# Optimization experiments

Hardware: AMD Instinct MI355X
Metric: run time of the kernel (lower is better)

The kernel has to match this reference:

```python
import jax, jax.numpy as jnp
import numpy as np

NUM_BANDS, B, K, D = 5, 512, 64, 200
H = 4            # num attention heads
HID = 512        # selector hidden width
S = 0.02         # weight init scale


def setup_inputs() -> dict:
    key = jax.random.key(0)
    ks = jax.random.split(key, 8)
    F_IN = NUM_BANDS * K * D  # 64000
    return {
        "bands": jax.random.normal(ks[0], (NUM_BANDS, B, K, D), jnp.float32),
        "w1": jax.random.normal(ks[1], (HID, F_IN), jnp.float32) * S,
        "b1": jnp.zeros((HID,), jnp.float32),
        "w2": jax.random.normal(ks[2], (NUM_BANDS, HID), jnp.float32) * S,
        "b2": jnp.zeros((NUM_BANDS,), jnp.float32),
        "in_proj_w": jax.random.normal(ks[3], (3 * D, D), jnp.float32) * S,
        "in_proj_b": jnp.zeros((3 * D,), jnp.float32),
        "out_w": jax.random.normal(ks[4], (D, D), jnp.float32) * S,
        "out_b": jnp.zeros((D,), jnp.float32),
    }


def reference(bands, w1, b1, w2, b2, in_proj_w, in_proj_b, out_w, out_b):
    nb, Bb, k, d = bands.shape
    hd = d // H
    scale = 1.0 / np.sqrt(hd)

    # concat(bands, dim=1): [B, nb*k, d] in band-major order
    x = jnp.transpose(bands, (1, 0, 2, 3))           # [B, nb, k, d]
    kv_in = x.reshape(Bb, nb * k, d)                 # [B, nb*k, d]

    # router MLP + softmax + argmax band select
    flat = kv_in.reshape(Bb, -1)                     # [B, nb*k*d]
    h = jax.nn.relu(flat @ w1.T + b1)                # [B, HID]
    band_weights = jax.nn.softmax(h @ w2.T + b2, axis=-1)
    sel = jnp.argmax(band_weights, axis=-1)          # [B] int

    # gather selected band per sample as the query
    Q = bands[sel, jnp.arange(Bb)]                   # [B, k, d]

    # multihead cross-attention (torch nn.MultiheadAttention math)
    wq, wk, wv = jnp.split(in_proj_w, 3, axis=0)
    bq, bk, bv = jnp.split(in_proj_b, 3, axis=0)
    q = (Q @ wq.T + bq).reshape(Bb, k, H, hd).transpose(0, 2, 1, 3)        # [B,H,k,hd]
    kk = (kv_in @ wk.T + bk).reshape(Bb, nb * k, H, hd).transpose(0, 2, 1, 3)
    v = (kv_in @ wv.T + bv).reshape(Bb, nb * k, H, hd).transpose(0, 2, 1, 3)

    attn = jax.nn.softmax(jnp.einsum('bhqe,bhke->bhqk', q, kk) * scale, axis=-1)
    o = jnp.einsum('bhqk,bhke->bhqe', attn, v)       # [B,H,k,hd]
    o = o.transpose(0, 2, 1, 3).reshape(Bb, k, d)
    return o @ out_w.T + out_b                        # [B, k, d]
```

## Files before the change

### kernel.cpp

```cpp
#include <hip/hip_runtime.h>
#include <hip/hip_bf16.h>

#define NBANDS 5
#define BATCH  512
#define KQN    64
#define DM     200
#define NHEAD  4
#define HD     50
#define HIDW   512
#define TKV    320
#define FIN    64000
#define BSTRIDE 6553600
#define KSPLIT 50
#define KCH    1280
#define NCH    40
#define NTT    13
#define KST    7
#define NTKV   25

typedef __bf16  bf16x8 __attribute__((ext_vector_type(8)));
typedef float   f32x4  __attribute__((ext_vector_type(4)));

static __device__ inline unsigned short f2bf(float f) {
    __hip_bfloat16 h = __float2bfloat16(f);
    return *reinterpret_cast<unsigned short*>(&h);
}
static __device__ inline float bf2f(unsigned short u) {
    union { unsigned int i; float f; } x;
    x.i = ((unsigned int)u) << 16;
    return x.f;
}
static __device__ inline bf16x8 bf8zero() {
    union { bf16x8 v; unsigned int u[4]; } z;
    z.u[0] = z.u[1] = z.u[2] = z.u[3] = 0u;
    return z.v;
}
static __device__ inline void split8(const float4& a, const float4& b,
                                     bf16x8& hi, bf16x8& lo) {
    union { bf16x8 v; unsigned short u[8]; } H, L;
    const float xs[8] = {a.x, a.y, a.z, a.w, b.x, b.y, b.z, b.w};
#pragma unroll
    for (int i = 0; i < 8; ++i) {
        H.u[i] = f2bf(xs[i]);
        L.u[i] = f2bf(xs[i] - bf2f(H.u[i]));
    }
    hi = H.v; lo = L.v;
}
static __device__ inline bf16x8 round8(const float4& a, const float4& b) {
    union { bf16x8 v; unsigned short u[8]; } H;
    const float xs[8] = {a.x, a.y, a.z, a.w, b.x, b.y, b.z, b.w};
#pragma unroll
    for (int i = 0; i < 8; ++i) H.u[i] = f2bf(xs[i]);
    return H.v;
}

__global__ __launch_bounds__(256) void k_splitw1(
    const float* __restrict__ w1, unsigned short* __restrict__ BHp,
    unsigned short* __restrict__ BLp)
{
    __shared__ __align__(16) unsigned short Hs[128][72];
    __shared__ __align__(16) unsigned short Ls[128][72];
    const int kc = blockIdx.x;
    const int jt = blockIdx.y;
    const int t  = threadIdx.x;
    const int rl0 = t >> 4, cl4 = (t & 15) * 4;
#pragma unroll
    for (int i = 0; i < 8; ++i) {
        const int row = rl0 + i * 16;
        const float4 v = *(const float4*)(w1
            + (size_t)(jt * 128 + row) * FIN + kc * 64 + cl4);
        ushort4 hh, ll;
        hh.x = f2bf(v.x); ll.x = f2bf(v.x - bf2f(hh.x));
        hh.y = f2bf(v.y); ll.y = f2bf(v.y - bf2f(hh.y));
        hh.z = f2bf(v.z); ll.z = f2bf(v.z - bf2f(hh.z));
        hh.w = f2bf(v.w); ll.w = f2bf(v.w - bf2f(hh.w));
        *(ushort4*)&Hs[row][cl4] = hh;
        *(ushort4*)&Ls[row][cl4] = ll;
    }
    __syncthreads();
    const size_t tbase = ((size_t)(jt * 1000 + kc)) << 13;
#pragma unroll
    for (int i = 0; i < 4; ++i) {
        const int slot = i * 256 + t;
        const int ksnt = slot >> 6, lane = slot & 63;
        const int ks = ksnt >> 3, nt = ksnt & 7;
        const int row = nt * 16 + (lane & 15);
        const int col = ks * 32 + (lane >> 4) * 8;
        *(uint4*)(BHp + tbase + (size_t)slot * 8) = *(const uint4*)&Hs[row][col];
        *(uint4*)(BLp + tbase + (size_t)slot * 8) = *(const uint4*)&Ls[row][col];
    }
}

__global__ __launch_bounds__(512, 2) void k_router_mfma(
    const float* __restrict__ bands, const unsigned short* __restrict__ BHp,
    const unsigned short* __restrict__ BLp, float* __restrict__ part)
{
    __shared__ __align__(16) unsigned short BsH[2][8192];
    __shared__ __align__(16) unsigned short BsL[2][8192];
    __shared__ __align__(16) unsigned short Ah[8192];
    __shared__ __align__(16) unsigned short Al[8192];

    const int lin = (blockIdx.z << 2) | (blockIdx.y << 1) | blockIdx.x;
    const int logical = (lin & 7) * 25 + (lin >> 3);
    const int z   = logical >> 2;
    const int rem = logical & 3;
    const int bt  = rem >> 1, jt = rem & 1;

    const int t = threadIdx.x;
    const int w = t >> 6, lane = t & 63;
    const int lm = lane & 15, quad = lane >> 4;
    const int wr = w >> 2, wc = w & 3;

    const float* abase = bands + (size_t)(z / 10) * BSTRIDE
                       + (size_t)(bt * 256 + w * 32 + lm) * 12800
                       + (z % 10) * KCH + quad * 8;

    auto stageB = [&](int c, int buf) {
        const int kc = z * 20 + (c >> 1);
        const int ks = c & 1;
#pragma unroll
        for (int p = 0; p < 4; ++p) {
            const int plane = p >> 1, r = p & 1;
            const unsigned short* src = (plane ? BLp : BHp)
                + ((size_t)((jt * 2 + r) * 1000 + kc) << 13) + (ks << 12)
                + (size_t)t * 8;
            unsigned short* dst = (plane ? &BsL[buf][0] : &BsH[buf][0])
                + (r << 12) + ((t >> 6) << 9);
            __builtin_amdgcn_global_load_lds(
                (const __attribute__((address_space(1))) unsigned int*)src,
                (__attribute__((address_space(3))) unsigned int*)dst, 16, 0, 0);
        }
    };

    float4 ar[4];
    auto loadA = [&](int c) {
        const float* ap = abase + c * 32;
        ar[0] = *(const float4*)(ap);
        ar[1] = *(const float4*)(ap + 4);
        ar[2] = *(const float4*)(ap + (size_t)16 * 12800);
        ar[3] = *(const float4*)(ap + (size_t)16 * 12800 + 4);
    };
    auto writeA = [&]() {
        bf16x8 h0, l0, h1, l1;
        split8(ar[0], ar[1], h0, l0);
        split8(ar[2], ar[3], h1, l1);
        *(bf16x8*)&Ah[(w * 2 + 0) * 512 + lane * 8] = h0;
        *(bf16x8*)&Al[(w * 2 + 0) * 512 + lane * 8] = l0;
        *(bf16x8*)&Ah[(w * 2 + 1) * 512 + lane * 8] = h1;
        *(bf16x8*)&Al[(w * 2 + 1) * 512 + lane * 8] = l1;
    };

    f32x4 acc[8][4];
#pragma unroll
    for (int rs = 0; rs < 8; ++rs)
#pragma unroll
        for (int nt = 0; nt < 4; ++nt) acc[rs][nt] = (f32x4){0.f, 0.f, 0.f, 0.f};

    loadA(0);
    stageB(0, 0);
    __syncthreads();
    writeA();
    __syncthreads();

    for (int c = 0; c < NCH; ++c) {
        if (c + 1 < NCH) {
            stageB(c + 1, (c + 1) & 1);
            loadA(c + 1);
        }
        const unsigned short* bh = &BsH[c & 1][(wc * 4) * 512 + lane * 8];
        const unsigned short* bl = &BsL[c & 1][(wc * 4) * 512 + lane * 8];
        const unsigned short* ahp = &Ah[(wr * 8) * 512 + lane * 8];
        const unsigned short* alp = &Al[(wr * 8) * 512 + lane * 8];
        bf16x8 bhv[4], blv[4];
#pragma unroll
        for (int nt = 0; nt < 4; ++nt) {
            bhv[nt] = *(const bf16x8*)(bh + nt * 512);
            blv[nt] = *(const bf16x8*)(bl + nt * 512);
        }
#pragma unroll
        for (int rs = 0; rs < 8; ++rs) {
            const bf16x8 a_h = *(const bf16x8*)(ahp + rs * 512);
            const bf16x8 a_l = *(const bf16x8*)(alp + rs * 512);
#pragma unroll
            for (int nt = 0; nt < 4; ++nt) {
                acc[rs][nt] = __builtin_amdgcn_mfma_f32_16x16x32_bf16(a_h, bhv[nt], acc[rs][nt], 0, 0, 0);
                acc[rs][nt] = __builtin_amdgcn_mfma_f32_16x16x32_bf16(a_l, bhv[nt], acc[rs][nt], 0, 0, 0);
                acc[rs][nt] = __builtin_amdgcn_mfma_f32_16x16x32_bf16(a_h, blv[nt], acc[rs][nt], 0, 0, 0);
            }
        }
        __syncthreads();
        if (c + 1 < NCH) {
            writeA();
        }
        __syncthreads();
    }

    float* po = part + (size_t)z * (BATCH * HIDW);
    const int j0 = jt * 256 + wc * 64;
    const int b0 = bt * 256 + wr * 128;
#pragma unroll
    for (int rs = 0; rs < 8; ++rs) {
#pragma unroll
        for (int nt = 0; nt < 4; ++nt) {
            const int jj = j0 + nt * 16 + lm;
#pragma unroll
            for (int reg = 0; reg < 4; ++reg) {
                const int bb = b0 + rs * 16 + quad * 4 + reg;
                po[(size_t)bb * HIDW + jj] = acc[rs][nt][reg];
            }
        }
    }
}

__global__ __launch_bounds__(256) void k_reduce_relu(
    const float* __restrict__ part, const float* __restrict__ b1,
    float* __restrict__ h)
{
    const int tid = blockIdx.x * 256 + threadIdx.x;
    float s = b1[tid & (HIDW - 1)];
#pragma unroll 10
    for (int z = 0; z < KSPLIT; ++z) s += part[z * (BATCH * HIDW) + tid];
    h[tid] = fmaxf(s, 0.f);
}

__global__ __launch_bounds__(256) void k_wpack(
    const float* __restrict__ ipw, const float* __restrict__ outw,
    unsigned short* __restrict__ WqHp, unsigned short* __restrict__ WqLp,
    unsigned short* __restrict__ OwHp, unsigned short* __restrict__ OwLp)
{
    const int p = blockIdx.x;
    const int ks = p / NTT, nt = p - ks * NTT;
    const int t = threadIdx.x;
    const int lane = t >> 2, e0 = (t & 3) * 2;
    const int lm = lane & 15, quad = lane >> 4;
    const int row = nt * 16 + lm;
    const int k  = ks * 32 + quad * 8 + e0;
    const float* src = (blockIdx.y == 0) ? ipw : outw;
    unsigned short* dh = (blockIdx.y == 0) ? WqHp : OwHp;
    unsigned short* dl = (blockIdx.y == 0) ? WqLp : OwLp;
    float v0 = 0.f, v1 = 0.f;
    if (row < DM && k < DM) {
        v0 = src[(size_t)row * DM + k];
        v1 = src[(size_t)row * DM + k + 1];
    }
    const int off = (p << 9) + (lane << 3) + e0;
    const unsigned short h0 = f2bf(v0), h1 = f2bf(v1);
    dh[off]     = h0;
    dh[off + 1] = h1;
    dl[off]     = f2bf(v0 - bf2f(h0));
    dl[off + 1] = f2bf(v1 - bf2f(h1));
}

__global__ __launch_bounds__(256) void k_wpack_kv(
    const float* __restrict__ ipw, unsigned short* __restrict__ Wkv)
{
    const int p = blockIdx.x;
    const int ks = p / NTKV, nt = p - ks * NTKV;
    const int t = threadIdx.x;
    const int lane = t >> 2, e0 = (t & 3) * 2;
    const int lm = lane & 15, quad = lane >> 4;
    const int row = nt * 16 + lm;
    const int k  = ks * 32 + quad * 8 + e0;
    float v0 = 0.f, v1 = 0.f;
    if (k < DM) {
        v0 = ipw[(size_t)(DM + row) * DM + k];
        v1 = ipw[(size_t)(DM + row) * DM + k + 1];
    }
    const int off = (p << 9) + (lane << 3) + e0;
    Wkv[off]     = f2bf(v0);
    Wkv[off + 1] = f2bf(v1);
}

__global__ __launch_bounds__(256) void k_argmax(
    const float* __restrict__ h, const float* __restrict__ w2,
    const float* __restrict__ b2, int* __restrict__ sel)
{
    __shared__ float red[NBANDS][256];
    const int b = blockIdx.x, t = threadIdx.x;
    float acc[NBANDS] = {0.f, 0.f, 0.f, 0.f, 0.f};
    for (int j = t; j < HIDW; j += 256) {
        const float hv = h[b * HIDW + j];
#pragma unroll
        for (int n = 0; n < NBANDS; ++n)
            acc[n] = fmaf(hv, w2[n * HIDW + j], acc[n]);
    }
#pragma unroll
    for (int n = 0; n < NBANDS; ++n) red[n][t] = acc[n];
    __syncthreads();
    for (int s = 128; s > 0; s >>= 1) {
        if (t < s) {
#pragma unroll
            for (int n = 0; n < NBANDS; ++n) red[n][t] += red[n][t + s];
        }
        __syncthreads();
    }
    if (t == 0) {
        int best = 0;
        float bv = red[0][0] + b2[0];
        for (int n = 1; n < NBANDS; ++n) {
            const float v = red[n][0] + b2[n];
            if (v > bv) { bv = v; best = n; }
        }
        sel[b] = best;
    }
}

template<bool BF16OUT>
static __device__ inline void proj_core(
    const float* __restrict__ x0,
    const unsigned short* __restrict__ Ph,
    const unsigned short* __restrict__ Pl,
    const float* __restrict__ bias,
    void* __restrict__ outp)
{
    const int t = threadIdx.x;
    const int w = t >> 6, lane = t & 63;
    const int lm = lane & 15, quad = lane >> 4;
    const int m0 = w * 16;
    const float* xrow = x0 + (size_t)(m0 + lm) * DM;

    f32x4 acc[NTT];
#pragma unroll
    for (int nt = 0; nt < NTT; ++nt) acc[nt] = (f32x4){0.f, 0.f, 0.f, 0.f};

#pragma unroll
    for (int ks = 0; ks < KST; ++ks) {
        const int k0 = ks * 32 + quad * 8;
        bf16x8 a_h = bf8zero(), a_l = bf8zero();
        if (k0 + 8 <= DM) {
            const float4 xa = *(const float4*)(xrow + k0);
            const float4 xb = *(const float4*)(xrow + k0 + 4);
            split8(xa, xb, a_h, a_l);
        }
        const unsigned short* ph = Ph + ((ks * NTT) << 9) + (lane << 3);
        const unsigned short* pl = Pl + ((ks * NTT) << 9) + (lane << 3);
#pragma unroll
        for (int nt = 0; nt < NTT; ++nt) {
            const bf16x8 b_h = *(const bf16x8*)(ph + (nt << 9));
            const bf16x8 b_l = *(const bf16x8*)(pl + (nt << 9));
            acc[nt] = __builtin_amdgcn_mfma_f32_16x16x32_bf16(a_h, b_h, acc[nt], 0, 0, 0);
            acc[nt] = __builtin_amdgcn_mfma_f32_16x16x32_bf16(a_l, b_h, acc[nt], 0, 0, 0);
            acc[nt] = __builtin_amdgcn_mfma_f32_16x16x32_bf16(a_h, b_l, acc[nt], 0, 0, 0);
        }
    }
#pragma unroll
    for (int nt = 0; nt < NTT; ++nt) {
        const int col = nt * 16 + lm;
        if (col < DM) {
            const float bs = bias[col];
#pragma unroll
            for (int reg = 0; reg < 4; ++reg) {
                const int row = m0 + quad * 4 + reg;
                const float v = acc[nt][reg] + bs;
                if (BF16OUT)
                    ((unsigned short*)outp)[(size_t)row * DM + col] = f2bf(v);
                else
                    ((float*)outp)[(size_t)row * DM + col] = v;
            }
        }
    }
}

__global__ __launch_bounds__(256) void k_qproj_mfma(
    const float* __restrict__ bands, const int* __restrict__ sel,
    const unsigned short* __restrict__ WqHp, const unsigned short* __restrict__ WqLp,
    const float* __restrict__ ipb, unsigned short* __restrict__ qb)
{
    const int b = blockIdx.x;
    const int band = sel[b];
    const float* x0 = bands + (size_t)((band * BATCH + b) * KQN) * DM;
    proj_core<true>(x0, WqHp, WqLp, ipb, qb + (size_t)(b * KQN) * DM);
}

__global__ __launch_bounds__(256) void k_outproj_mfma(
    const float* __restrict__ obuf, const unsigned short* __restrict__ OwHp,
    const unsigned short* __restrict__ OwLp, const float* __restrict__ outb,
    float* __restrict__ out)
{
    const int b = blockIdx.x;
    proj_core<false>(obuf + (size_t)(b * KQN) * DM, OwHp, OwLp, outb,
                     out + (size_t)(b * KQN) * DM);
}

__global__ __launch_bounds__(256) void k_kvproj_lds(
    const float* __restrict__ bands, const unsigned short* __restrict__ Wkv,
    const float* __restrict__ ipb, __hip_bfloat16* __restrict__ Kp,
    __hip_bfloat16* __restrict__ Vp)
{
    __shared__ __align__(16) unsigned short Bs[2][NTKV * 512];
    const int t = threadIdx.x;
    const int w = t >> 6, lane = t & 63;
    const int lm = lane & 15, quad = lane >> 4;
    const int m0 = w * 16;
    const int M0 = blockIdx.x * 64;

    const int gg = M0 + m0 + lm;
    const int bb = gg / TKV, tk = gg - bb * TKV;
    const int band = tk >> 6, kk = tk & 63;
    const float* xrow = bands + (size_t)((band * BATCH + bb) * KQN + kk) * DM;

    float4 ar[2 * KST];
#pragma unroll
    for (int ks = 0; ks < KST; ++ks) {
        const int k0 = ks * 32 + quad * 8;
        if (k0 + 8 <= DM) {
            ar[2 * ks]     = *(const float4*)(xrow + k0);
            ar[2 * ks + 1] = *(const float4*)(xrow + k0 + 4);
        }
    }
    bf16x8 a[KST];
#pragma unroll
    for (int ks = 0; ks < KST; ++ks) {
        const int k0 = ks * 32 + quad * 8;
        a[ks] = (k0 + 8 <= DM) ? round8(ar[2 * ks], ar[2 * ks + 1]) : bf8zero();
    }

    auto stage = [&](int ks, int buf) {
        const unsigned short* src = Wkv + ((ks * NTKV) << 9);
#pragma unroll
        for (int pass = 0; pass < 6; ++pass) {
            const int i = pass * 256 + t;
            __builtin_amdgcn_global_load_lds(
                (const __attribute__((address_space(1))) unsigned int*)(src + (size_t)i * 8),
                (__attribute__((address_space(3))) unsigned int*)&Bs[buf][(pass * 256 + w * 64) * 8],
                16, 0, 0);
        }
        if (t < 64) {
            __builtin_amdgcn_global_load_lds(
                (const __attribute__((address_space(1))) unsigned int*)(src + (size_t)(1536 + lane) * 8),
                (__attribute__((address_space(3))) unsigned int*)&Bs[buf][1536 * 8],
                16, 0, 0);
        }
    };

    f32x4 acc[NTKV];
#pragma unroll
    for (int nt = 0; nt < NTKV; ++nt) acc[nt] = (f32x4){0.f, 0.f, 0.f, 0.f};

    stage(0, 0);
    __syncthreads();
#pragma unroll
    for (int ks = 0; ks < KST; ++ks) {
        if (ks + 1 < KST) stage(ks + 1, (ks + 1) & 1);
        const unsigned short* bs = &Bs[ks & 1][lane * 8];
#pragma unroll
        for (int nt = 0; nt < NTKV; ++nt) {
            const bf16x8 b8 = *(const bf16x8*)(bs + (nt << 9));
            acc[nt] = __builtin_amdgcn_mfma_f32_16x16x32_bf16(a[ks], b8, acc[nt], 0, 0, 0);
        }
        __syncthreads();
    }

#pragma unroll
    for (int nt = 0; nt < NTKV; ++nt) {
        const int col = nt * 16 + lm;
        const float bias = ipb[DM + col];
#pragma unroll
        for (int reg = 0; reg < 4; ++reg) {
            const int grow = M0 + m0 + quad * 4 + reg;
            const float v = acc[nt][reg] + bias;
            if (col < DM) Kp[(size_t)grow * DM + col] = __float2bfloat16(v);
            else          Vp[(size_t)grow * DM + (col - DM)] = __float2bfloat16(v);
        }
    }
}

__global__ __launch_bounds__(256) void k_attn(
    const unsigned short* __restrict__ qb, const __hip_bfloat16* __restrict__ Kp,
    const __hip_bfloat16* __restrict__ Vp, float* __restrict__ obuf)
{
    __shared__ __align__(16) unsigned short Qs[64][72];
    __shared__ __align__(16) unsigned short KP[320][72];
    __shared__ __align__(16) unsigned short Vt[64][328];
    __shared__ __align__(16) unsigned short Ps[64][328];
    const int b = blockIdx.x, hh = blockIdx.y;
    const int t = threadIdx.x;

    const unsigned short* qbase = qb + (size_t)(b * KQN) * DM + hh * HD;
    for (int idx = t; idx < 64 * 64; idx += 256) {
        const int r = idx >> 6, e = idx & 63;
        Qs[r][e] = (e < HD) ? qbase[(size_t)r * DM + e] : 0;
    }
    const unsigned short* kbase = (const unsigned short*)Kp + (size_t)b * TKV * DM + hh * HD;
    for (int idx = t; idx < 320 * 25; idx += 256) {
        const int key = idx / 25, g = idx - key * 25;
        *(unsigned int*)&KP[key][g * 2] =
            *(const unsigned int*)(kbase + (size_t)key * DM + g * 2);
    }
    for (int idx = t; idx < 320 * 7; idx += 256) {
        const int key = idx / 7, g = idx - key * 7;
        *(unsigned int*)&KP[key][50 + g * 2] = 0;
    }
    const unsigned short* vbase = (const unsigned short*)Vp + (size_t)b * TKV * DM + hh * HD;
    for (int idx = t; idx < 320 * 25; idx += 256) {
        const int key = idx / 25, g = idx - key * 25;
        const unsigned int v = *(const unsigned int*)(vbase + (size_t)key * DM + g * 2);
        Vt[g * 2][key]     = (unsigned short)(v & 0xffffu);
        Vt[g * 2 + 1][key] = (unsigned short)(v >> 16);
    }
    __syncthreads();

    const int w = t >> 6, lane = t & 63;
    const int lm = lane & 15, quad = lane >> 4;
    const int m0 = w * 16;

    f32x4 s[20];
#pragma unroll
    for (int nt = 0; nt < 20; ++nt) s[nt] = (f32x4){0.f, 0.f, 0.f, 0.f};
#pragma unroll
    for (int ks = 0; ks < 2; ++ks) {
        const int ka = ks * 32 + quad * 8;
        const bf16x8 a = *(const bf16x8*)&Qs[m0 + lm][ka];
#pragma unroll
        for (int nt = 0; nt < 20; ++nt) {
            const bf16x8 bb8 = *(const bf16x8*)&KP[nt * 16 + lm][ka];
            s[nt] = __builtin_amdgcn_mfma_f32_16x16x32_bf16(a, bb8, s[nt], 0, 0, 0);
        }
    }

    const float scale = 0.14142135623730951f;
    float inv[4];
#pragma unroll
    for (int reg = 0; reg < 4; ++reg) {
        float mx = -1e30f;
#pragma unroll
        for (int nt = 0; nt < 20; ++nt) {
            const float sv = s[nt][reg] * scale;
            s[nt][reg] = sv;
            mx = fmaxf(mx, sv);
        }
#pragma unroll
        for (int off = 1; off < 16; off <<= 1)
            mx = fmaxf(mx, __shfl_xor(mx, off, 64));
        float lsum = 0.f;
#pragma unroll
        for (int nt = 0; nt < 20; ++nt) {
            const float p = __expf(s[nt][reg] - mx);
            s[nt][reg] = p;
            lsum += p;
        }
#pragma unroll
        for (int off = 1; off < 16; off <<= 1)
            lsum += __shfl_xor(lsum, off, 64);
        inv[reg] = 1.f / lsum;
    }
#pragma unroll
    for (int reg = 0; reg < 4; ++reg) {
        const int row = m0 + quad * 4 + reg;
#pragma unroll
        for (int nt = 0; nt < 20; ++nt)
            Ps[row][nt * 16 + lm] = f2bf(s[nt][reg]);
    }
    __syncthreads();

    f32x4 o[4];
#pragma unroll
    for (int nt = 0; nt < 4; ++nt) o[nt] = (f32x4){0.f, 0.f, 0.f, 0.f};
#pragma unroll
    for (int ks = 0; ks < 10; ++ks) {
        const int ka = ks * 32 + quad * 8;
        const bf16x8 a = *(const bf16x8*)&Ps[m0 + lm][ka];
#pragma unroll
        for (int nt = 0; nt < 4; ++nt) {
            const bf16x8 bb8 = *(const bf16x8*)&Vt[nt * 16 + lm][ka];
            o[nt] = __builtin_amdgcn_mfma_f32_16x16x32_bf16(a, bb8, o[nt], 0, 0, 0);
        }
    }
    float* op = obuf + (size_t)(b * KQN) * DM + hh * HD;
#pragma unroll
    for (int nt = 0; nt < 4; ++nt) {
        const int e = nt * 16 + lm;
        if (e < HD) {
#pragma unroll
            for (int reg = 0; reg < 4; ++reg) {
                const int row = m0 + quad * 4 + reg;
                op[(size_t)row * DM + e] = o[nt][reg] * inv[reg];
            }
        }
    }
}

extern "C" void kernel_launch(void* const* d_in, const int* in_sizes, int n_in,
                              void* d_out, int out_size, void* d_ws, size_t ws_size,
                              hipStream_t stream)
{
    const float* bands = (const float*)d_in[0];
    const float* w1    = (const float*)d_in[1];
    const float* b1    = (const float*)d_in[2];
    const float* w2    = (const float*)d_in[3];
    const float* b2    = (const float*)d_in[4];
    const float* ipw   = (const float*)d_in[5];
    const float* ipb   = (const float*)d_in[6];
    const float* outw  = (const float*)d_in[7];
    const float* outb  = (const float*)d_in[8];
    float* out = (float*)d_out;

    if (ws_size < (size_t)192940032) return;

    char* ws = (char*)d_ws;
    int*   sel  = (int*)  (ws + 0);
    unsigned short* BHp  = (unsigned short*)(ws + 4096);
    unsigned short* BLp  = (unsigned short*)(ws + 65540096);
    float* part = (float*)(ws + 131076096);
    float* h    = (float*)(ws + 183504896);
    unsigned short* qb   = (unsigned short*)(ws + 4096);
    __hip_bfloat16* Kp   = (__hip_bfloat16*)(ws + 26776832);
    __hip_bfloat16* Vp   = (__hip_bfloat16*)(ws + 92312832);
    float* obuf = (float*)(ws + 157848832);
    unsigned short* Wkv  = (unsigned short*)(ws + 184553472);
    unsigned short* WqHp = (unsigned short*)(ws + 184732672);
    unsigned short* WqLp = (unsigned short*)(ws + 184825856);
    unsigned short* OwHp = (unsigned short*)(ws + 184919040);
    unsigned short* OwLp = (unsigned short*)(ws + 185012224);

    k_wpack_kv<<<KST * NTKV, 256, 0, stream>>>(ipw, Wkv);
    k_wpack<<<dim3(KST * NTT, 2), 256, 0, stream>>>(ipw, outw, WqHp, WqLp, OwHp, OwLp);
    k_splitw1<<<dim3(1000, 4), 256, 0, stream>>>(w1, BHp, BLp);

    k_router_mfma<<<dim3(2, 2, KSPLIT), 512, 0, stream>>>(bands, BHp, BLp, part);
    k_reduce_relu<<<(BATCH * HIDW) / 256, 256, 0, stream>>>(part, b1, h);
    k_argmax<<<BATCH, 256, 0, stream>>>(h, w2, b2, sel);
    k_qproj_mfma<<<BATCH, 256, 0, stream>>>(bands, sel, WqHp, WqLp, ipb, qb);
    k_kvproj_lds<<<2560, 256, 0, stream>>>(bands, Wkv, ipb, Kp, Vp);
    k_attn<<<dim3(BATCH, NHEAD), 256, 0, stream>>>(qb, Kp, Vp, obuf);
    k_outproj_mfma<<<BATCH, 256, 0, stream>>>(obuf, OwHp, OwLp, outb, out);
}
```

Baseline: 813.0 us.

## Halve router GEMM batch tile to 128 rows and raise occupancy

Shrinks the router MFMA block's batch tile from 256 to 128 rows, which doubles the grid and halves the accumulator registers and A-tile shared memory. Launch bounds go from 2 to 4 blocks per CU, and the loop is reordered to load the A fragments once and stream B per column tile. The A split into bf16 hi/lo now happens at load time, and one barrier is dropped from the last iteration. In exchange, each W1 tile is fetched by twice as many blocks, which adds L2/HBM traffic for the weight operand.

```diff
diff --git a/kernel.cpp b/kernel.cpp
--- a/kernel.cpp
+++ b/kernel.cpp
@@ -91,19 +91,19 @@
     }
 }
 
-__global__ __launch_bounds__(512, 2) void k_router_mfma(
+__global__ __launch_bounds__(512, 4) void k_router_mfma(
     const float* __restrict__ bands, const unsigned short* __restrict__ BHp,
     const unsigned short* __restrict__ BLp, float* __restrict__ part)
 {
     __shared__ __align__(16) unsigned short BsH[2][8192];
     __shared__ __align__(16) unsigned short BsL[2][8192];
-    __shared__ __align__(16) unsigned short Ah[8192];
-    __shared__ __align__(16) unsigned short Al[8192];
-
-    const int lin = (blockIdx.z << 2) | (blockIdx.y << 1) | blockIdx.x;
-    const int logical = (lin & 7) * 25 + (lin >> 3);
-    const int z   = logical >> 2;
-    const int rem = logical & 3;
+    __shared__ __align__(16) unsigned short Ah[4096];
+    __shared__ __align__(16) unsigned short Al[4096];
+
+    const int lin = (blockIdx.z << 3) | (blockIdx.y << 1) | blockIdx.x;
+    const int logical = (lin & 7) * 50 + (lin >> 3);
+    const int z   = logical >> 3;
+    const int rem = logical & 7;
     const int bt  = rem >> 1, jt = rem & 1;
 
     const int t = threadIdx.x;
@@ -112,7 +112,7 @@
     const int wr = w >> 2, wc = w & 3;
 
     const float* abase = bands + (size_t)(z / 10) * BSTRIDE
-                       + (size_t)(bt * 256 + w * 32 + lm) * 12800
+                       + (size_t)(bt * 128 + w * 16 + lm) * 12800
                        + (z % 10) * KCH + quad * 8;
 
     auto stageB = [&](int c, int buf) {
@@ -120,86 +120,83 @@
         const int ks = c & 1;
 #pragma unroll
         for (int p = 0; p < 4; ++p) {
-            const int plane = p >> 1, r = p & 1;
+            const int plane = p >> 1, oj = p & 1;
             const unsigned short* src = (plane ? BLp : BHp)
-                + ((size_t)((jt * 2 + r) * 1000 + kc) << 13) + (ks << 12)
+                + ((size_t)((jt * 2 + oj) * 1000 + kc) << 13) + (ks << 12)
                 + (size_t)t * 8;
             unsigned short* dst = (plane ? &BsL[buf][0] : &BsH[buf][0])
-                + (r << 12) + ((t >> 6) << 9);
+                + (oj << 12) + (w << 9);
             __builtin_amdgcn_global_load_lds(
                 (const __attribute__((address_space(1))) unsigned int*)src,
                 (__attribute__((address_space(3))) unsigned int*)dst, 16, 0, 0);
         }
     };
 
-    float4 ar[4];
-    auto loadA = [&](int c) {
+    bf16x8 ahn, aln;
+    auto loadsplitA = [&](int c) {
         const float* ap = abase + c * 32;
-        ar[0] = *(const float4*)(ap);
-        ar[1] = *(const float4*)(ap + 4);
-        ar[2] = *(const float4*)(ap + (size_t)16 * 12800);
-        ar[3] = *(const float4*)(ap + (size_t)16 * 12800 + 4);
+        const float4 x0 = *(const float4*)(ap);
+        const float4 x1 = *(const float4*)(ap + 4);
+        split8(x0, x1, ahn, aln);
     };
     auto writeA = [&]() {
-        bf16x8 h0, l0, h1, l1;
-        split8(ar[0], ar[1], h0, l0);
-        split8(ar[2], ar[3], h1, l1);
-        *(bf16x8*)&Ah[(w * 2 + 0) * 512 + lane * 8] = h0;
-        *(bf16x8*)&Al[(w * 2 + 0) * 512 + lane * 8] = l0;
-        *(bf16x8*)&Ah[(w * 2 + 1) * 512 + lane * 8] = h1;
-        *(bf16x8*)&Al[(w * 2 + 1) * 512 + lane * 8] = l1;
+        *(bf16x8*)&Ah[w * 512 + lane * 8] = ahn;
+        *(bf16x8*)&Al[w * 512 + lane * 8] = aln;
     };
 
-    f32x4 acc[8][4];
-#pragma unroll
-    for (int rs = 0; rs < 8; ++rs)
+    f32x4 acc[4][4];
+#pragma unroll
+    for (int rs = 0; rs < 4; ++rs)
 #pragma unroll
         for (int nt = 0; nt < 4; ++nt) acc[rs][nt] = (f32x4){0.f, 0.f, 0.f, 0.f};
 
-    loadA(0);
+    loadsplitA(0);
     stageB(0, 0);
-    __syncthreads();
     writeA();
     __syncthreads();
 
+    const unsigned short* hbase = &BsH[0][((wc >> 1) << 12) + ((wc & 1) * 4) * 512 + lane * 8];
+    const unsigned short* lbase = &BsL[0][((wc >> 1) << 12) + ((wc & 1) * 4) * 512 + lane * 8];
+    const unsigned short* ahp = &Ah[(wr * 4) * 512 + lane * 8];
+    const unsigned short* alp = &Al[(wr * 4) * 512 + lane * 8];
+
     for (int c = 0; c < NCH; ++c) {
+        const int buf = c & 1;
         if (c + 1 < NCH) {
-            stageB(c + 1, (c + 1) & 1);
-            loadA(c + 1);
-        }
-        const unsigned short* bh = &BsH[c & 1][(wc * 4) * 512 + lane * 8];
-        const unsigned short* bl = &BsL[c & 1][(wc * 4) * 512 + lane * 8];
-        const unsigned short* ahp = &Ah[(wr * 8) * 512 + lane * 8];
-        const unsigned short* alp = &Al[(wr * 8) * 512 + lane * 8];
-        bf16x8 bhv[4], blv[4];
+            stageB(c + 1, buf ^ 1);
+            loadsplitA(c + 1);
+        }
+        const unsigned short* hc = hbase + buf * 8192;
+        const unsigned short* lc = lbase + buf * 8192;
+        bf16x8 af[4], alf[4];
+#pragma unroll
+        for (int rs = 0; rs < 4; ++rs) {
+            af[rs]  = *(const bf16x8*)(ahp + rs * 512);
+            alf[rs] = *(const bf16x8*)(alp + rs * 512);
+        }
 #pragma unroll
         for (int nt = 0; nt < 4; ++nt) {
-            bhv[nt] = *(const bf16x8*)(bh + nt * 512);
-            blv[nt] = *(const bf16x8*)(bl + nt * 512);
-        }
-#pragma unroll
-        for (int rs = 0; rs < 8; ++rs) {
-            const bf16x8 a_h = *(const bf16x8*)(ahp + rs * 512);
-            const bf16x8 a_l = *(const bf16x8*)(alp + rs * 512);
-#pragma unroll
-            for (int nt = 0; nt < 4; ++nt) {
-                acc[rs][nt] = __builtin_amdgcn_mfma_f32_16x16x32_bf16(a_h, bhv[nt], acc[rs][nt], 0, 0, 0);
-                acc[rs][nt] = __builtin_amdgcn_mfma_f32_16x16x32_bf16(a_l, bhv[nt], acc[rs][nt], 0, 0, 0);
-                acc[rs][nt] = __builtin_amdgcn_mfma_f32_16x16x32_bf16(a_h, blv[nt], acc[rs][nt], 0, 0, 0);
+            const bf16x8 bh = *(const bf16x8*)(hc + nt * 512);
+            const bf16x8 bl = *(const bf16x8*)(lc + nt * 512);
+#pragma unroll
+            for (int rs = 0; rs < 4; ++rs) {
+                acc[rs][nt] = __builtin_amdgcn_mfma_f32_16x16x32_bf16(af[rs], bh, acc[rs][nt], 0, 0, 0);
+                acc[rs][nt] = __builtin_amdgcn_mfma_f32_16x16x32_bf16(alf[rs], bh, acc[rs][nt], 0, 0, 0);
+                acc[rs][nt] = __builtin_amdgcn_mfma_f32_16x16x32_bf16(af[rs], bl, acc[rs][nt], 0, 0, 0);
             }
         }
         __syncthreads();
         if (c + 1 < NCH) {
             writeA();
-        }
-        __syncthreads();
+            __syncthreads();
+        }
     }
 
     float* po = part + (size_t)z * (BATCH * HIDW);
     const int j0 = jt * 256 + wc * 64;
-    const int b0 = bt * 256 + wr * 128;
-#pragma unroll
-    for (int rs = 0; rs < 8; ++rs) {
+    const int b0 = bt * 128 + wr * 64;
+#pragma unroll
+    for (int rs = 0; rs < 4; ++rs) {
 #pragma unroll
         for (int nt = 0; nt < 4; ++nt) {
             const int jj = j0 + nt * 16 + lm;
@@ -617,7 +614,7 @@
     k_wpack<<<dim3(KST * NTT, 2), 256, 0, stream>>>(ipw, outw, WqHp, WqLp, OwHp, OwLp);
     k_splitw1<<<dim3(1000, 4), 256, 0, stream>>>(w1, BHp, BLp);
 
-    k_router_mfma<<<dim3(2, 2, KSPLIT), 512, 0, stream>>>(bands, BHp, BLp, part);
+    k_router_mfma<<<dim3(2, 4, KSPLIT), 512, 0, stream>>>(bands, BHp, BLp, part);
     k_reduce_relu<<<(BATCH * HIDW) / 256, 256, 0, stream>>>(part, b1, h);
     k_argmax<<<BATCH, 256, 0, stream>>>(h, w2, b2, sel);
     k_qproj_mfma<<<BATCH, 256, 0, stream>>>(bands, sel, WqHp, WqLp, ipb, qb);
```

Result: no change. 800.3 us (-1.6%).
